# Kernel optimization log

Hardware: AMD Instinct MI355X
Metric: run time of the kernel (lower is better)

The kernel has to match this reference:

```python
import jax, jax.numpy as jnp
import numpy as np

DIM = 1024
HEADS = 16
HEAD_DIM = DIM // HEADS
SCALE = HEAD_DIM ** -0.5


def setup_inputs() -> dict:
    key = jax.random.key(0)
    ks = jax.random.split(key, 6)
    B, N = 2, 2048
    s = DIM ** -0.5
    return {
        "x": jax.random.normal(ks[0], (B, N, DIM), dtype=jnp.float32),
        "Wq": jax.random.normal(ks[1], (DIM, DIM), dtype=jnp.float32) * s,
        "Wk": jax.random.normal(ks[2], (DIM, DIM), dtype=jnp.float32) * s,
        "Wv": jax.random.normal(ks[3], (DIM, DIM), dtype=jnp.float32) * s,
        "Wo": jax.random.normal(ks[4], (DIM, DIM), dtype=jnp.float32) * s,
        "bo": jnp.zeros((DIM,), dtype=jnp.float32),
    }


def reference(x, Wq, Wk, Wv, Wo, bo):
    B, N, D = x.shape
    # Linear projections (torch Linear: y = x @ W.T)
    q = x @ Wq.T
    k = x @ Wk.T
    v = x @ Wv.T
    # [B, H, N, hd]
    q = q.reshape(B, N, HEADS, HEAD_DIM).transpose(0, 2, 1, 3)
    k = k.reshape(B, N, HEADS, HEAD_DIM).transpose(0, 2, 1, 3)
    v = v.reshape(B, N, HEADS, HEAD_DIM).transpose(0, 2, 1, 3)
    scores = jnp.einsum('bhid,bhjd->bhij', q, k) * SCALE
    probs = jax.nn.softmax(scores, axis=-1)
    out = jnp.einsum('bhij,bhjd->bhid', probs, v)
    out = out.transpose(0, 2, 1, 3).reshape(B, N, D)
    return out @ Wo.T + bo
```

## Files before the change

kernel.cpp:

```cpp
#include <hip/hip_runtime.h>

#define DIM    1024
#define HEADS  16
#define HD     64
#define BATCH  2
#define SEQ    2048
#define C2     0.18033688011112042f

typedef __attribute__((ext_vector_type(8))) short           short8;
typedef __attribute__((ext_vector_type(4))) short           short4v;
typedef __attribute__((ext_vector_type(4))) float           f4;
typedef __attribute__((ext_vector_type(4))) unsigned short  u16x4;
typedef __attribute__((ext_vector_type(4))) unsigned int    u32x4;
typedef __attribute__((ext_vector_type(2))) unsigned int    u32x2;

typedef __attribute__((address_space(3))) unsigned int       as3_u32;
typedef const __attribute__((address_space(1))) unsigned int as1_u32;

__device__ __forceinline__ unsigned short f2bf(float f) {
    unsigned int u = __builtin_bit_cast(unsigned int, f);
    u = (u + 0x7fffu + ((u >> 16) & 1u)) >> 16;
    return (unsigned short)u;
}
__device__ __forceinline__ unsigned int pk_bf16(float a, float b) {
    return (unsigned int)f2bf(a) | ((unsigned int)f2bf(b) << 16);
}

#if __has_builtin(__builtin_amdgcn_exp2f)
#define EXP2(x) __builtin_amdgcn_exp2f(x)
#else
#define EXP2(x) exp2f(x)
#endif

__device__ __forceinline__ void gl2lds16(const unsigned short* g, unsigned short* l) {
    __builtin_amdgcn_global_load_lds((as1_u32*)g, (as3_u32*)l, 16, 0, 0);
}

__global__ __launch_bounds__(256) void k_cast_all(
    const float* __restrict__ x,  const float* __restrict__ wq,
    const float* __restrict__ wk, const float* __restrict__ wv,
    const float* __restrict__ wo, unsigned short* __restrict__ dst)
{
    const int i = blockIdx.x * 256 + threadIdx.x;
    const float* src;
    int off;
    if (i < (1 << 20))            { src = x;  off = 0; }
    else if (i < (5 << 18))       { src = wq; off = 1 << 20; }
    else if (i < (6 << 18))       { src = wk; off = 5 << 18; }
    else if (i < (7 << 18))       { src = wv; off = 6 << 18; }
    else                          { src = wo; off = 7 << 18; }
    f4 v = ((const f4*)src)[i - off];
    u16x4 o;
    o[0] = f2bf(v[0]); o[1] = f2bf(v[1]); o[2] = f2bf(v[2]); o[3] = f2bf(v[3]);
    ((u16x4*)dst)[i] = o;
}

__global__ __launch_bounds__(256) void gemm_qkv(
    const unsigned short* __restrict__ A,
    const unsigned short* __restrict__ Wq,
    const unsigned short* __restrict__ Wk,
    const unsigned short* __restrict__ Wv,
    unsigned short* __restrict__ Qo,
    unsigned short* __restrict__ Ko,
    unsigned short* __restrict__ Vo)
{
    __shared__ __align__(16) unsigned short Xs[128 * 32];
    __shared__ __align__(16) unsigned short Ws[128 * 32];
    const int L   = blockIdx.x;
    const int xcd = L & 7;
    const int idx = L >> 3;
    const int col = idx >> 2;
    const int sb  = (xcd * 4 + (idx & 3)) * 128;
    const int wsel = col >> 3;
    const int fb   = (col & 7) * 128;
    const unsigned short* W = (wsel == 0) ? Wq : ((wsel == 1) ? Wk : Wv);

    const int tid  = threadIdx.x;
    const int wave = tid >> 6, lane = tid & 63;
    const int quad = lane >> 4, l16 = lane & 15;
    const int wm = (wave & 1) << 6, wn = (wave >> 1) << 6;

    const unsigned short* aLDS = (wsel < 2) ? Ws : Xs;
    const unsigned short* bLDS = (wsel < 2) ? Xs : Ws;

    f4 acc[4][4] = {};

    for (int k0 = 0; k0 < DIM; k0 += 32) {
        __syncthreads();
        #pragma unroll
        for (int i = 0; i < 2; i++) {
            const int c = tid + (i << 8);
            const int row = c >> 2, koff = (c & 3) << 3;
            gl2lds16(&A[(size_t)(sb + row) * DIM + k0 + koff], &Xs[(size_t)((i << 8) + (wave << 6)) * 8]);
            gl2lds16(&W[(size_t)(fb + row) * DIM + k0 + koff], &Ws[(size_t)((i << 8) + (wave << 6)) * 8]);
        }
        __syncthreads();
        short8 afr[4], bfr[4];
        #pragma unroll
        for (int i = 0; i < 4; i++)
            afr[i] = *(const short8*)(&aLDS[(wm + i * 16 + l16) * 32 + quad * 8]);
        #pragma unroll
        for (int j = 0; j < 4; j++)
            bfr[j] = *(const short8*)(&bLDS[(wn + j * 16 + l16) * 32 + quad * 8]);
        #pragma unroll
        for (int i = 0; i < 4; i++)
            #pragma unroll
            for (int j = 0; j < 4; j++)
                acc[i][j] = __builtin_amdgcn_mfma_f32_16x16x32_bf16(afr[i], bfr[j], acc[i][j], 0, 0, 0);
    }

    if (wsel < 2) {
        unsigned short* out = (wsel == 0) ? Qo : Ko;
        const float sc = (wsel == 0) ? C2 : 1.0f;
        #pragma unroll
        for (int j = 0; j < 4; j++) {
            const int ms = sb + wn + j * 16 + l16;
            const int b = ms >> 11, ns = ms & (SEQ - 1);
            #pragma unroll
            for (int i = 0; i < 4; i++) {
                const int feat = fb + wm + i * 16 + quad * 4;
                const int h = feat >> 6, d = feat & (HD - 1);
                u32x2 pw;
                pw[0] = pk_bf16(acc[i][j][0] * sc, acc[i][j][1] * sc);
                pw[1] = pk_bf16(acc[i][j][2] * sc, acc[i][j][3] * sc);
                *(u32x2*)(&out[((size_t)(b * HEADS + h) * SEQ + ns) * HD + d]) = pw;
            }
        }
    } else {
        #pragma unroll
        for (int j = 0; j < 4; j++) {
            const int feat = fb + wn + j * 16 + l16;
            const int h = feat >> 6, d = feat & (HD - 1);
            #pragma unroll
            for (int i = 0; i < 4; i++) {
                const int ms = sb + wm + i * 16 + quad * 4;
                const int b = ms >> 11, ns = ms & (SEQ - 1);
                u32x2 pw;
                pw[0] = pk_bf16(acc[i][j][0], acc[i][j][1]);
                pw[1] = pk_bf16(acc[i][j][2], acc[i][j][3]);
                *(u32x2*)(&Vo[((size_t)(b * HEADS + h) * HD + d) * SEQ + ns]) = pw;
            }
        }
    }
}

__global__ __launch_bounds__(256) void attn_fwd(
    const unsigned short* __restrict__ Qg,
    const unsigned short* __restrict__ Kg,
    const unsigned short* __restrict__ VTg,
    unsigned short* __restrict__ AOb)
{
    __shared__ __align__(16) unsigned short QsP[128 * 72];
    __shared__ __align__(16) unsigned short Ks [64 * 72];
    __shared__ __align__(16) unsigned short VsT[64 * 72];

    const int L   = blockIdx.x;
    const int xcd = L & 7;
    const int idx = L >> 3;
    const int bh  = xcd * 4 + (idx >> 4);
    const int q0  = (idx & 15) << 7;

    const unsigned short* Qb  = Qg  + (size_t)bh * SEQ * HD;
    const unsigned short* Kb  = Kg  + (size_t)bh * SEQ * HD;
    const unsigned short* VTb = VTg + (size_t)bh * HD * SEQ;

    const int tid  = threadIdx.x;
    const int wave = tid >> 6, lane = tid & 63;
    const int quad = lane >> 4, l16 = lane & 15;
    const int qw   = wave << 5;
    const int r8   = tid >> 3;
    const int g8   = (tid & 7) * 8;

    #pragma unroll
    for (int p = 0; p < 4; p++) {
        const int row = r8 + p * 32;
        *(u32x4*)(&QsP[row * 72 + g8]) = *(const u32x4*)(&Qb[(size_t)(q0 + row) * HD + g8]);
    }
    #pragma unroll
    for (int p = 0; p < 2; p++) {
        const int row = r8 + p * 32;
        *(u32x4*)(&Ks [row * 72 + g8]) = *(const u32x4*)(&Kb [(size_t)row * HD + g8]);
        *(u32x4*)(&VsT[row * 72 + g8]) = *(const u32x4*)(&VTb[(size_t)row * SEQ + g8]);
    }
    __syncthreads();

    short8 qf[2][2];
    #pragma unroll
    for (int nf = 0; nf < 2; nf++)
        #pragma unroll
        for (int ks = 0; ks < 2; ks++)
            qf[nf][ks] = *(const short8*)(&QsP[(qw + nf * 16 + l16) * 72 + ks * 32 + quad * 8]);

    f4 lsum[2] = {};
    f4 Oacc[4][2] = {};

    for (int kt = 0; kt < SEQ / 64; kt++) {
        u32x4 kpre[2], vpre[2];
        if (kt < SEQ / 64 - 1) {
            #pragma unroll
            for (int p = 0; p < 2; p++) {
                const int row = r8 + p * 32;
                kpre[p] = *(const u32x4*)(&Kb [(size_t)((kt + 1) * 64 + row) * HD + g8]);
                vpre[p] = *(const u32x4*)(&VTb[(size_t)row * SEQ + (kt + 1) * 64 + g8]);
            }
        }

        f4 sacc[4][2] = {};
        #pragma unroll
        for (int ks = 0; ks < 2; ks++) {
            short8 kfr[4];
            #pragma unroll
            for (int mf = 0; mf < 4; mf++)
                kfr[mf] = *(const short8*)(&Ks[(mf * 16 + l16) * 72 + ks * 32 + quad * 8]);
            #pragma unroll
            for (int mf = 0; mf < 4; mf++)
                #pragma unroll
                for (int nf = 0; nf < 2; nf++)
                    sacc[mf][nf] = __builtin_amdgcn_mfma_f32_16x16x32_bf16(kfr[mf], qf[nf][ks], sacc[mf][nf], 0, 0, 0);
        }

#if __has_builtin(__builtin_amdgcn_mfma_f32_16x16x16bf16_1k)
        short4v pb[2][4];
        #pragma unroll
        for (int nf = 0; nf < 2; nf++) {
            #pragma unroll
            for (int mf = 0; mf < 4; mf++) {
                f4 pv;
                #pragma unroll
                for (int r = 0; r < 4; r++)
                    pv[r] = EXP2(sacc[mf][nf][r]);
                lsum[nf] += pv;
                short4v pk;
                #pragma unroll
                for (int r = 0; r < 4; r++)
                    pk[r] = (short)f2bf(pv[r]);
                pb[nf][mf] = pk;
            }
        }
        #pragma unroll
        for (int ks16 = 0; ks16 < 4; ks16++) {
            short4v vfr[4];
            #pragma unroll
            for (int mf = 0; mf < 4; mf++)
                vfr[mf] = *(const short4v*)(&VsT[(mf * 16 + l16) * 72 + ks16 * 16 + quad * 4]);
            #pragma unroll
            for (int mf = 0; mf < 4; mf++)
                #pragma unroll
                for (int nf = 0; nf < 2; nf++)
                    Oacc[mf][nf] = __builtin_amdgcn_mfma_f32_16x16x16bf16_1k(vfr[mf], pb[nf][ks16], Oacc[mf][nf], 0, 0, 0);
        }
#else
        #pragma unroll
        for (int nf = 0; nf < 2; nf++) {
            #pragma unroll
            for (int mf = 0; mf < 4; mf++) {
                f4 pv;
                #pragma unroll
                for (int r = 0; r < 4; r++)
                    pv[r] = EXP2(sacc[mf][nf][r]);
                lsum[nf] += pv;
                u32x2 pw;
                pw[0] = pk_bf16(pv[0], pv[1]);
                pw[1] = pk_bf16(pv[2], pv[3]);
                *(u32x2*)(&QsP[(qw + nf * 16 + l16) * 72 + mf * 16 + quad * 4]) = pw;
            }
        }
        #pragma unroll
        for (int ks = 0; ks < 2; ks++) {
            short8 vfr[4], pf[2];
            #pragma unroll
            for (int mf = 0; mf < 4; mf++)
                vfr[mf] = *(const short8*)(&VsT[(mf * 16 + l16) * 72 + ks * 32 + quad * 8]);
            #pragma unroll
            for (int nf = 0; nf < 2; nf++)
                pf[nf] = *(const short8*)(&QsP[(qw + nf * 16 + l16) * 72 + ks * 32 + quad * 8]);
            #pragma unroll
            for (int mf = 0; mf < 4; mf++)
                #pragma unroll
                for (int nf = 0; nf < 2; nf++)
                    Oacc[mf][nf] = __builtin_amdgcn_mfma_f32_16x16x32_bf16(vfr[mf], pf[nf], Oacc[mf][nf], 0, 0, 0);
        }
#endif

        __syncthreads();
        if (kt < SEQ / 64 - 1) {
            #pragma unroll
            for (int p = 0; p < 2; p++) {
                const int row = r8 + p * 32;
                *(u32x4*)(&Ks [row * 72 + g8]) = kpre[p];
                *(u32x4*)(&VsT[row * 72 + g8]) = vpre[p];
            }
        }
        __syncthreads();
    }

    const int b = bh >> 4, h = bh & (HEADS - 1);
    #pragma unroll
    for (int nf = 0; nf < 2; nf++) {
        float l = lsum[nf][0] + lsum[nf][1] + lsum[nf][2] + lsum[nf][3];
        l += __shfl_xor(l, 16);
        l += __shfl_xor(l, 32);
        const float inv = 1.0f / l;
        const int qg = q0 + qw + nf * 16 + l16;
        #pragma unroll
        for (int mf = 0; mf < 4; mf++) {
            u32x2 o;
            o[0] = pk_bf16(Oacc[mf][nf][0] * inv, Oacc[mf][nf][1] * inv);
            o[1] = pk_bf16(Oacc[mf][nf][2] * inv, Oacc[mf][nf][3] * inv);
            *(u32x2*)(&AOb[(size_t)(b * SEQ + qg) * DIM + h * HD + mf * 16 + quad * 4]) = o;
        }
    }
}

__global__ __launch_bounds__(256) void gemm_out(
    const unsigned short* __restrict__ AO,
    const unsigned short* __restrict__ W,
    float* __restrict__ out,
    const float* __restrict__ bias)
{
    __shared__ __align__(16) unsigned short As[64 * 32];
    __shared__ __align__(16) unsigned short Bs[128 * 32];
    const int L   = blockIdx.x;
    const int xcd = L & 7;
    const int idx = L >> 3;
    const int n0  = (xcd * 4 + (idx >> 4)) * 128;
    const int m0  = (idx & 15) * 64;

    const int tid  = threadIdx.x;
    const int wave = tid >> 6, lane = tid & 63;
    const int quad = lane >> 4, l16 = lane & 15;
    const int wm = (wave & 1) << 5, wn = (wave >> 1) << 6;

    f4 acc[2][4] = {};

    for (int k0 = 0; k0 < DIM; k0 += 32) {
        __syncthreads();
        gl2lds16(&W[(size_t)(m0 + (tid >> 2)) * DIM + k0 + ((tid & 3) << 3)],
                 &As[(size_t)(wave << 6) * 8]);
        #pragma unroll
        for (int i = 0; i < 2; i++) {
            const int c = tid + (i << 8);
            gl2lds16(&AO[(size_t)(n0 + (c >> 2)) * DIM + k0 + ((c & 3) << 3)],
                     &Bs[(size_t)((i << 8) + (wave << 6)) * 8]);
        }
        __syncthreads();
        short8 afr[2], bfr[4];
        #pragma unroll
        for (int i = 0; i < 2; i++)
            afr[i] = *(const short8*)(&As[(wm + i * 16 + l16) * 32 + quad * 8]);
        #pragma unroll
        for (int j = 0; j < 4; j++)
            bfr[j] = *(const short8*)(&Bs[(wn + j * 16 + l16) * 32 + quad * 8]);
        #pragma unroll
        for (int i = 0; i < 2; i++)
            #pragma unroll
            for (int j = 0; j < 4; j++)
                acc[i][j] = __builtin_amdgcn_mfma_f32_16x16x32_bf16(afr[i], bfr[j], acc[i][j], 0, 0, 0);
    }

    #pragma unroll
    for (int i = 0; i < 2; i++) {
        const int feat = m0 + wm + i * 16 + quad * 4;
        const f4 bv = *(const f4*)(&bias[feat]);
        #pragma unroll
        for (int j = 0; j < 4; j++) {
            const int ns = n0 + wn + j * 16 + l16;
            *(f4*)(&out[(size_t)ns * DIM + feat]) = acc[i][j] + bv;
        }
    }
}

extern "C" void kernel_launch(void* const* d_in, const int* in_sizes, int n_in,
                              void* d_out, int out_size, void* d_ws, size_t ws_size,
                              hipStream_t stream) {
    (void)in_sizes; (void)n_in; (void)out_size; (void)ws_size;
    const float* x  = (const float*)d_in[0];
    const float* Wq = (const float*)d_in[1];
    const float* Wk = (const float*)d_in[2];
    const float* Wv = (const float*)d_in[3];
    const float* Wo = (const float*)d_in[4];
    const float* bo = (const float*)d_in[5];

    unsigned short* wsu = (unsigned short*)d_ws;
    unsigned short* xb  = wsu;
    unsigned short* Wqb = wsu + (4u  << 20);
    unsigned short* Wkb = wsu + (5u  << 20);
    unsigned short* Wvb = wsu + (6u  << 20);
    unsigned short* Wob = wsu + (7u  << 20);
    unsigned short* Qb  = wsu + (8u  << 20);
    unsigned short* Kb  = wsu + (12u << 20);
    unsigned short* VTb = wsu + (16u << 20);
    unsigned short* AOb = wsu + (20u << 20);

    k_cast_all<<<8192, 256, 0, stream>>>(x, Wq, Wk, Wv, Wo, wsu);

    gemm_qkv<<<768, 256, 0, stream>>>(xb, Wqb, Wkb, Wvb, Qb, Kb, VTb);

    attn_fwd<<<512, 256, 0, stream>>>(Qb, Kb, VTb, AOb);

    gemm_out<<<512, 256, 0, stream>>>(AOb, Wob, (float*)d_out, bo);
}
```

Measured before the change: 191.9 us.

## Split attention key range into two halves and merge partials in a combine kernel

The attention kernel now launches twice as many blocks, each covering half of the key sequence. Each block writes its unnormalized bf16 partial output and its row sums into workspace buffers, reusing regions that are dead at that point. A new k_combine kernel adds the two partials and divides by the combined sum before gemm_out runs. The aim is more blocks to fill the GPU and more latency hiding, at the cost of an extra launch, extra global traffic for the partial buffers, and an added bf16 rounding of the unnormalized partials.

```diff
diff --git a/kernel.cpp b/kernel.cpp
--- a/kernel.cpp
+++ b/kernel.cpp
@@ -24,6 +24,12 @@
 }
 __device__ __forceinline__ unsigned int pk_bf16(float a, float b) {
     return (unsigned int)f2bf(a) | ((unsigned int)f2bf(b) << 16);
+}
+__device__ __forceinline__ float bf_lo(unsigned int u) {
+    return __builtin_bit_cast(float, u << 16);
+}
+__device__ __forceinline__ float bf_hi(unsigned int u) {
+    return __builtin_bit_cast(float, u & 0xffff0000u);
 }
 
 #if __has_builtin(__builtin_amdgcn_exp2f)
@@ -148,17 +154,21 @@
     const unsigned short* __restrict__ Qg,
     const unsigned short* __restrict__ Kg,
     const unsigned short* __restrict__ VTg,
-    unsigned short* __restrict__ AOb)
+    unsigned short* __restrict__ Op0,
+    unsigned short* __restrict__ Op1,
+    float* __restrict__ Lp)
 {
     __shared__ __align__(16) unsigned short QsP[128 * 72];
     __shared__ __align__(16) unsigned short Ks [64 * 72];
     __shared__ __align__(16) unsigned short VsT[64 * 72];
 
-    const int L   = blockIdx.x;
-    const int xcd = L & 7;
-    const int idx = L >> 3;
-    const int bh  = xcd * 4 + (idx >> 4);
-    const int q0  = (idx & 15) << 7;
+    const int L     = blockIdx.x;
+    const int xcd   = L & 7;
+    const int idx   = L >> 3;
+    const int bh    = xcd * 4 + (idx >> 5);
+    const int split = (idx >> 4) & 1;
+    const int q0    = (idx & 15) << 7;
+    const int kt0   = split * 16;
 
     const unsigned short* Qb  = Qg  + (size_t)bh * SEQ * HD;
     const unsigned short* Kb  = Kg  + (size_t)bh * SEQ * HD;
@@ -179,8 +189,8 @@
     #pragma unroll
     for (int p = 0; p < 2; p++) {
         const int row = r8 + p * 32;
-        *(u32x4*)(&Ks [row * 72 + g8]) = *(const u32x4*)(&Kb [(size_t)row * HD + g8]);
-        *(u32x4*)(&VsT[row * 72 + g8]) = *(const u32x4*)(&VTb[(size_t)row * SEQ + g8]);
+        *(u32x4*)(&Ks [row * 72 + g8]) = *(const u32x4*)(&Kb [(size_t)(kt0 * 64 + row) * HD + g8]);
+        *(u32x4*)(&VsT[row * 72 + g8]) = *(const u32x4*)(&VTb[(size_t)row * SEQ + kt0 * 64 + g8]);
     }
     __syncthreads();
 
@@ -194,9 +204,9 @@
     f4 lsum[2] = {};
     f4 Oacc[4][2] = {};
 
-    for (int kt = 0; kt < SEQ / 64; kt++) {
+    for (int kt = kt0; kt < kt0 + 16; kt++) {
         u32x4 kpre[2], vpre[2];
-        if (kt < SEQ / 64 - 1) {
+        if (kt < kt0 + 15) {
             #pragma unroll
             for (int p = 0; p < 2; p++) {
                 const int row = r8 + p * 32;
@@ -283,7 +293,7 @@
 #endif
 
         __syncthreads();
-        if (kt < SEQ / 64 - 1) {
+        if (kt < kt0 + 15) {
             #pragma unroll
             for (int p = 0; p < 2; p++) {
                 const int row = r8 + p * 32;
@@ -294,22 +304,50 @@
         __syncthreads();
     }
 
+    unsigned short* Od = split ? Op1 : Op0;
     const int b = bh >> 4, h = bh & (HEADS - 1);
     #pragma unroll
     for (int nf = 0; nf < 2; nf++) {
         float l = lsum[nf][0] + lsum[nf][1] + lsum[nf][2] + lsum[nf][3];
         l += __shfl_xor(l, 16);
         l += __shfl_xor(l, 32);
-        const float inv = 1.0f / l;
         const int qg = q0 + qw + nf * 16 + l16;
+        if (quad == 0)
+            Lp[((size_t)split * 32 + bh) * SEQ + qg] = l;
         #pragma unroll
         for (int mf = 0; mf < 4; mf++) {
             u32x2 o;
-            o[0] = pk_bf16(Oacc[mf][nf][0] * inv, Oacc[mf][nf][1] * inv);
-            o[1] = pk_bf16(Oacc[mf][nf][2] * inv, Oacc[mf][nf][3] * inv);
-            *(u32x2*)(&AOb[(size_t)(b * SEQ + qg) * DIM + h * HD + mf * 16 + quad * 4]) = o;
-        }
-    }
+            o[0] = pk_bf16(Oacc[mf][nf][0], Oacc[mf][nf][1]);
+            o[1] = pk_bf16(Oacc[mf][nf][2], Oacc[mf][nf][3]);
+            *(u32x2*)(&Od[(size_t)(b * SEQ + qg) * DIM + h * HD + mf * 16 + quad * 4]) = o;
+        }
+    }
+}
+
+__global__ __launch_bounds__(256) void k_combine(
+    const unsigned short* __restrict__ O0,
+    const unsigned short* __restrict__ O1,
+    const float* __restrict__ Lp,
+    unsigned short* __restrict__ AOb)
+{
+    const int idx = blockIdx.x * 256 + threadIdx.x;
+    const int e = idx << 3;
+    const int row = e >> 10;
+    const int col = e & 1023;
+    const int b = row >> 11, q = row & (SEQ - 1), h = col >> 6;
+    const size_t lidx = (size_t)(b * HEADS + h) * SEQ + q;
+    const float inv = 1.0f / (Lp[lidx] + Lp[(size_t)32 * SEQ + lidx]);
+
+    const u32x4 a = ((const u32x4*)O0)[idx];
+    const u32x4 c = ((const u32x4*)O1)[idx];
+    u32x4 o;
+    #pragma unroll
+    for (int i = 0; i < 4; i++) {
+        const float lo = (bf_lo(a[i]) + bf_lo(c[i])) * inv;
+        const float hi = (bf_hi(a[i]) + bf_hi(c[i])) * inv;
+        o[i] = pk_bf16(lo, hi);
+    }
+    ((u32x4*)AOb)[idx] = o;
 }
 
 __global__ __launch_bounds__(256) void gemm_out(
@@ -392,11 +430,17 @@
     unsigned short* VTb = wsu + (16u << 20);
     unsigned short* AOb = wsu + (20u << 20);
 
+    unsigned short* Op0 = AOb;
+    unsigned short* Op1 = xb;
+    float*          Lp  = (float*)Wqb;
+
     k_cast_all<<<8192, 256, 0, stream>>>(x, Wq, Wk, Wv, Wo, wsu);
 
     gemm_qkv<<<768, 256, 0, stream>>>(xb, Wqb, Wkb, Wvb, Qb, Kb, VTb);
 
-    attn_fwd<<<512, 256, 0, stream>>>(Qb, Kb, VTb, AOb);
+    attn_fwd<<<1024, 256, 0, stream>>>(Qb, Kb, VTb, Op0, Op1, Lp);
+
+    k_combine<<<2048, 256, 0, stream>>>(Op0, Op1, Lp, AOb);
 
     gemm_out<<<512, 256, 0, stream>>>(AOb, Wob, (float*)d_out, bo);
 }
```

Measured after the change: 194.3 us. About the same (+1.3%).
